# Kernel optimization log

Measured on AMD Instinct MI355X. Metric: run time of the kernel, lower is better.

## Reference

```python
import jax, jax.numpy as jnp
import numpy as np

B, N, TF, DM = 16, 4096, 512, 1024

def next_fast_len(n):
    # smallest 5-smooth number >= n (matches scipy.fftpack.next_fast_len)
    while True:
        m = n
        for p in (2, 3, 5):
            while m % p == 0:
                m //= p
        if m == 1:
            return n
        n += 1

def conv1d_fft(x, weights):
    # x: (..., N, F), weights: (M,); causal exponentially-weighted correlation
    n = x.shape[-2]
    m = weights.shape[-1]
    L = next_fast_len(n + m - 1)
    f_x = jnp.fft.rfft(x, n=L, axis=-2)                 # (..., Lr, F) complex
    f_w = jnp.fft.rfft(weights, n=L, axis=-1)           # (Lr,)
    out = jnp.fft.irfft(f_x * jnp.conj(f_w)[..., None], L, axis=-2)
    out = jnp.roll(out, -1, axis=-2)
    return out[..., L - n:, :]                           # last N along seq axis

def setup_inputs() -> dict:
    key = jax.random.key(0)
    ks = jax.random.split(key, 8)
    inp = {
        "x": jax.random.normal(ks[0], (B, N, TF), dtype=jnp.float32),
        "latent_growth": jax.random.normal(ks[1], (B, N, DM), dtype=jnp.float32),
        "latent_seasonal": jax.random.normal(ks[2], (B, N, DM), dtype=jnp.float32),
        "alpha": jnp.zeros((1,), dtype=jnp.float32),  # nn.Parameter(torch.Tensor([0.0]))
        "w_growth": jax.random.normal(ks[3], (TF, DM), dtype=jnp.float32) / np.sqrt(DM),
        "b_growth": jnp.zeros((TF,), dtype=jnp.float32),
        "w_seasonal": jax.random.normal(ks[4], (TF, DM), dtype=jnp.float32) / np.sqrt(DM),
        "b_seasonal": jnp.zeros((TF,), dtype=jnp.float32),
    }
    return inp

def reference(x, latent_growth, latent_seasonal, alpha, w_growth, b_growth, w_seasonal, b_seasonal):
    n = x.shape[1]
    a = jax.nn.sigmoid(alpha)[0]
    powers = jnp.arange(n, dtype=x.dtype)[::-1]          # flipped arange
    seasonal = jnp.einsum('bnd,fd->bnf', latent_seasonal, w_seasonal) + b_seasonal
    aes_weights = a * (1.0 - a) ** powers                # alpha*(1-alpha)^k EMA kernel
    seasonal_normalized_term = conv1d_fft(x - seasonal, aes_weights)
    # NOTE: the original module computes `growth` but does not use it in the output
    growth = jnp.einsum('bnd,fd->bnf', latent_growth, w_growth) + b_growth
    growth_term = conv1d_fft(x, aes_weights)
    return seasonal_normalized_term + growth_term
```

## Files before the change

### kernel.cpp

```cpp
#include <hip/hip_runtime.h>
#include <math.h>

#define B_DIM 16
#define N_SEQ 4096
#define TF_DIM 512
#define DM_DIM 1024
#define CHUNK 128
#define NCHUNK (N_SEQ / CHUNK)
#define NKT (DM_DIM / 32)

typedef __attribute__((ext_vector_type(4))) float f32x4;
typedef __attribute__((ext_vector_type(8))) short bf16x8;
typedef unsigned short u16;
typedef unsigned int u32;

__device__ __forceinline__ u16 f2bf(float f) {
    u32 u = __builtin_bit_cast(u32, f);
    u += 0x7fffu + ((u >> 16) & 1u);
    return (u16)(u >> 16);
}

__device__ __forceinline__ u32 cvtpk(float lo, float hi) {
    u32 r;
    asm("v_cvt_pk_bf16_f32 %0, %1, %2" : "=v"(r) : "v"(lo), "v"(hi));
    return r;
}

__device__ __forceinline__ void gload16(const u16* g, u16* l) {
    __builtin_amdgcn_global_load_lds(
        (const __attribute__((address_space(1))) void*)g,
        (__attribute__((address_space(3))) void*)l, 16, 0, 0);
}

#define SYNC_DRAIN() asm volatile("s_waitcnt vmcnt(0)\n\ts_barrier" ::: "memory")

__global__ __launch_bounds__(256)
void cvt_bf16(const float* __restrict__ ls, const float* __restrict__ wm,
              u16* __restrict__ lsb, u16* __restrict__ wmb)
{
    const size_t LSG = (size_t)B_DIM * N_SEQ * DM_DIM / 4;
    const size_t i = (size_t)blockIdx.x * 256 + threadIdx.x;
    const float* src;
    u16* dst;
    if (i < LSG) { src = ls + i * 4; dst = lsb + i * 4; }
    else         { const size_t j = i - LSG; src = wm + j * 4; dst = wmb + j * 4; }
    const f32x4 v = *(const f32x4*)src;
    u32* d = (u32*)dst;
    d[0] = cvtpk(v[0], v[1]);
    d[1] = cvtpk(v[2], v[3]);
}

__global__ __launch_bounds__(512, 4)
void gemm_u_kernel(const float* __restrict__ x,
                   const u16* __restrict__ lsb,
                   const u16* __restrict__ wmb,
                   const float* __restrict__ bias,
                   const float* __restrict__ alpha,
                   u16* __restrict__ u,
                   float* __restrict__ e)
{
    __shared__ u16 As[2][8192];
    __shared__ u16 Ws[2][4096];
    __shared__ float red[2][2][4][16];

    const int tid = threadIdx.x;

    const int s  = blockIdx.x;
    const int kk = s >> 3;
    const int fb = kk & 3;
    const int rp = (s & 7) + ((kk >> 2) << 3);
    const int f0   = fb * 128;
    const int row0 = rp * 256;

    const int lane = tid & 63;
    const int wid  = tid >> 6;
    const int wm = wid >> 1, wn = wid & 1;
    const int l15 = lane & 15, l4 = lane >> 4;

    const int srow = lane >> 2;
    const int sgc  = (lane & 3) ^ (srow & 3);
    const u16* pA = lsb + (size_t)(row0 + wid * 32 + srow) * DM_DIM + sgc * 8;
    const u16* pW = wmb + (size_t)(f0 + wid * 16 + srow) * DM_DIM + sgc * 8;

#define STAGE(BUF, KT) do {                                              \
        const int _o = (KT) * 32;                                        \
        gload16(pA + _o,                 &As[BUF][wid * 1024]);          \
        gload16(pA + _o + 16 * DM_DIM,   &As[BUF][wid * 1024 + 512]);    \
        gload16(pW + _o,                 &Ws[BUF][wid * 512]);           \
    } while (0)

    int rofa[4], rofw[4];
#pragma unroll
    for (int i = 0; i < 4; ++i) {
        const int ra = wm * 64 + i * 16 + l15;
        const int rw = wn * 64 + i * 16 + l15;
        rofa[i] = ra * 32 + ((l4 ^ (ra & 3)) * 8);
        rofw[i] = rw * 32 + ((l4 ^ (rw & 3)) * 8);
    }

    f32x4 acc[4][4];
#pragma unroll
    for (int i = 0; i < 4; ++i)
#pragma unroll
        for (int j = 0; j < 4; ++j) acc[i][j] = (f32x4){0.f, 0.f, 0.f, 0.f};

#define COMPUTE(BUF) do {                                                \
        const u16* _Ab = As[BUF];                                        \
        const u16* _Wb = Ws[BUF];                                        \
        bf16x8 _af[4], _wf[4];                                           \
        _Pragma("unroll")                                                \
        for (int i = 0; i < 4; ++i) {                                    \
            _af[i] = *(const bf16x8*)(_Ab + rofa[i]);                    \
            _wf[i] = *(const bf16x8*)(_Wb + rofw[i]);                    \
        }                                                                \
        _Pragma("unroll")                                                \
        for (int mi = 0; mi < 4; ++mi)                                   \
        _Pragma("unroll")                                                \
        for (int ni = 0; ni < 4; ++ni)                                   \
            acc[mi][ni] = __builtin_amdgcn_mfma_f32_16x16x32_bf16(       \
                _af[mi], _wf[ni], acc[mi][ni], 0, 0, 0);                 \
    } while (0)

    STAGE(0, 0);
    SYNC_DRAIN();

#pragma unroll 1
    for (int kt = 0; kt < NKT; kt += 2) {
        if (kt + 1 < NKT) STAGE(1, kt + 1);
        COMPUTE(0);
        SYNC_DRAIN();

        if (kt + 2 < NKT) STAGE(0, kt + 2);
        COMPUTE(1);
        SYNC_DRAIN();
    }

    const float a = 1.0f / (1.0f + expf(-alpha[0]));
    const float c = 1.0f - a;
    const float l2c = log2f(c);

    float bia[4];
#pragma unroll
    for (int ni = 0; ni < 4; ++ni) bia[ni] = bias[f0 + wn * 64 + ni * 16 + l15];

    float epart[4] = {0.f, 0.f, 0.f, 0.f};

#pragma unroll
    for (int mi = 0; mi < 4; ++mi) {
#pragma unroll
        for (int j = 0; j < 4; ++j) {
            const int r = wm * 64 + mi * 16 + l4 * 4 + j;
            const int rc = r & (CHUNK - 1);
            const size_t rb = (size_t)(row0 + r) * TF_DIM;
            const float wgt = (rc == CHUNK - 1)
                                  ? a
                                  : a * exp2f((float)(CHUNK - 1 - rc) * l2c);
#pragma unroll
            for (int ni = 0; ni < 4; ++ni) {
                const int f = f0 + wn * 64 + ni * 16 + l15;
                const float uval = 2.0f * x[rb + f] - (acc[mi][ni][j] + bia[ni]);
                u[rb + f] = f2bf(uval);
                epart[ni] = fmaf(wgt, uval, epart[ni]);
            }
        }
    }

#pragma unroll
    for (int ni = 0; ni < 4; ++ni) {
        epart[ni] += __shfl_xor(epart[ni], 16, 64);
        epart[ni] += __shfl_xor(epart[ni], 32, 64);
    }
    const int ch = wm >> 1;
    if ((wm & 1) == 1 && l4 == 0) {
#pragma unroll
        for (int ni = 0; ni < 4; ++ni) red[ch][wn][ni][l15] = epart[ni];
    }
    __syncthreads();
    if ((wm & 1) == 0 && l4 == 0) {
#pragma unroll
        for (int ni = 0; ni < 4; ++ni) {
            const int f = f0 + wn * 64 + ni * 16 + l15;
            e[(size_t)(rp * 2 + ch) * TF_DIM + f] = epart[ni] + red[ch][wn][ni][l15];
        }
    }
}

__global__ __launch_bounds__(256)
void ema_carry(const float* __restrict__ e, const float* __restrict__ alpha,
               float* __restrict__ carry)
{
    const int idx = blockIdx.x * 256 + threadIdx.x;
    const int f = idx & (TF_DIM - 1);
    const int b = idx >> 9;
    const float a = 1.0f / (1.0f + expf(-alpha[0]));
    const float c = 1.0f - a;
    const float cC = exp2f((float)CHUNK * log2f(c));
    const size_t base = (size_t)b * NCHUNK * TF_DIM + f;
    float Y = 0.0f;
    carry[base] = 0.0f;
    for (int ch = 1; ch < NCHUNK; ++ch) {
        Y = fmaf(cC, Y, e[base + (size_t)(ch - 1) * TF_DIM]);
        carry[base + (size_t)ch * TF_DIM] = Y;
    }
}

__global__ __launch_bounds__(256)
void ema_apply(const u16* __restrict__ u, const float* __restrict__ carry,
               const float* __restrict__ alpha, float* __restrict__ out)
{
    const int bc = blockIdx.x;
    const int tid = threadIdx.x;
    const float a = 1.0f / (1.0f + expf(-alpha[0]));
    const float c = 1.0f - a;
    float y0 = carry[(size_t)bc * TF_DIM + 2 * tid];
    float y1 = carry[(size_t)bc * TF_DIM + 2 * tid + 1];
    const u32* up = (const u32*)(u + (size_t)bc * CHUNK * TF_DIM) + tid;
    float2*    op = (float2*)(out + (size_t)bc * CHUNK * TF_DIM) + tid;
#pragma unroll 4
    for (int j = 0; j < CHUNK; ++j) {
        const u32 w = up[(size_t)j * (TF_DIM / 2)];
        const float u0 = __builtin_bit_cast(float, (w & 0xffffu) << 16);
        const float u1 = __builtin_bit_cast(float, (w >> 16) << 16);
        y0 = fmaf(c, y0, a * u0);
        y1 = fmaf(c, y1, a * u1);
        op[(size_t)j * (TF_DIM / 2)] = make_float2(y0, y1);
    }
}

extern "C" void kernel_launch(void* const* d_in, const int* in_sizes, int n_in,
                              void* d_out, int out_size, void* d_ws, size_t ws_size,
                              hipStream_t stream) {
    const float* x     = (const float*)d_in[0];
    const float* ls    = (const float*)d_in[2];
    const float* alpha = (const float*)d_in[3];
    const float* wmat  = (const float*)d_in[6];
    const float* bias  = (const float*)d_in[7];
    float* out = (float*)d_out;

    u16*   u     = (u16*)d_ws;
    u16*   lsb   = u + (size_t)B_DIM * N_SEQ * TF_DIM;
    u16*   wmb   = lsb + (size_t)B_DIM * N_SEQ * DM_DIM;
    float* e     = (float*)(wmb + (size_t)TF_DIM * DM_DIM);
    float* carry = e + (size_t)B_DIM * NCHUNK * TF_DIM;

    const int cvt_blocks = (B_DIM * N_SEQ * DM_DIM / 4 + TF_DIM * DM_DIM / 4) / 256;
    cvt_bf16<<<cvt_blocks, 256, 0, stream>>>(ls, wmat, lsb, wmb);

    gemm_u_kernel<<<1024, 512, 0, stream>>>(x, lsb, wmb, bias, alpha, u, e);

    ema_carry<<<(B_DIM * TF_DIM) / 256, 256, 0, stream>>>(e, alpha, carry);
    ema_apply<<<B_DIM * NCHUNK, 256, 0, stream>>>(u, carry, alpha, out);
}
```

Before: 244.4 us.

## Enlarge GEMM tile to 256x256 with K=64 stages and split-phase pipelining

The seasonal GEMM block tile grows from 256x128 to 256x256, with each wave computing 128x64 (8x4 MFMA tiles), and the K step doubles to 64, so the grid drops to 512 blocks. The aim is more operand reuse per byte loaded from LDS and global memory, fewer barriers per K, and better MFMA density. Staging of A and W is split across sub-phases with s_setprio around the MFMA bursts to overlap loads with compute. The epilogue reduction no longer goes through shared memory because each wave now covers a full 128-row chunk. The cost is higher register and LDS use (64KB), which lowers occupancy to 2 blocks per CU.

```diff
diff --git a/kernel.cpp b/kernel.cpp
--- a/kernel.cpp
+++ b/kernel.cpp
@@ -7,7 +7,7 @@
 #define DM_DIM 1024
 #define CHUNK 128
 #define NCHUNK (N_SEQ / CHUNK)
-#define NKT (DM_DIM / 32)
+#define NT 16
 
 typedef __attribute__((ext_vector_type(4))) float f32x4;
 typedef __attribute__((ext_vector_type(8))) short bf16x8;
@@ -32,6 +32,7 @@
         (__attribute__((address_space(3))) void*)l, 16, 0, 0);
 }
 
+#define BAR() __builtin_amdgcn_s_barrier()
 #define SYNC_DRAIN() asm volatile("s_waitcnt vmcnt(0)\n\ts_barrier" ::: "memory")
 
 __global__ __launch_bounds__(256)
@@ -50,7 +51,7 @@
     d[1] = cvtpk(v[2], v[3]);
 }
 
-__global__ __launch_bounds__(512, 4)
+__global__ __launch_bounds__(512, 2)
 void gemm_u_kernel(const float* __restrict__ x,
                    const u16* __restrict__ lsb,
                    const u16* __restrict__ wmb,
@@ -59,79 +60,100 @@
                    u16* __restrict__ u,
                    float* __restrict__ e)
 {
-    __shared__ u16 As[2][8192];
-    __shared__ u16 Ws[2][4096];
-    __shared__ float red[2][2][4][16];
+    __shared__ u16 As[2][2][8192];
+    __shared__ u16 Ws[2][2][8192];
 
     const int tid = threadIdx.x;
 
     const int s  = blockIdx.x;
     const int kk = s >> 3;
-    const int fb = kk & 3;
-    const int rp = (s & 7) + ((kk >> 2) << 3);
-    const int f0   = fb * 128;
+    const int fb = kk & 1;
+    const int rp = (s & 7) + ((kk >> 1) << 3);
+    const int f0   = fb * 256;
     const int row0 = rp * 256;
 
     const int lane = tid & 63;
     const int wid  = tid >> 6;
-    const int wm = wid >> 1, wn = wid & 1;
+    const int wm = wid >> 2;
+    const int wn = wid & 3;
+    const int wh = wn >> 1, wlo = wn & 1;
     const int l15 = lane & 15, l4 = lane >> 4;
 
-    const int srow = lane >> 2;
-    const int sgc  = (lane & 3) ^ (srow & 3);
-    const u16* pA = lsb + (size_t)(row0 + wid * 32 + srow) * DM_DIM + sgc * 8;
-    const u16* pW = wmb + (size_t)(f0 + wid * 16 + srow) * DM_DIM + sgc * 8;
-
-#define STAGE(BUF, KT) do {                                              \
-        const int _o = (KT) * 32;                                        \
-        gload16(pA + _o,                 &As[BUF][wid * 1024]);          \
-        gload16(pA + _o + 16 * DM_DIM,   &As[BUF][wid * 1024 + 512]);    \
-        gload16(pW + _o,                 &Ws[BUF][wid * 512]);           \
+    const int g0 = wid * 128 + lane;
+    const int g1 = g0 + 64;
+    const int r0 = ((g0 >> 7) << 4) | ((g0 >> 2) & 15);
+    const int c0 = (((g0 >> 6) & 1) << 5) | ((((g0 & 3) ^ (((g0 >> 5) & 1) << 1))) << 3);
+    const int r1 = ((g1 >> 7) << 4) | ((g1 >> 2) & 15);
+    const int c1 = (((g1 >> 6) & 1) << 5) | ((((g1 & 3) ^ (((g1 >> 5) & 1) << 1))) << 3);
+    const int dst0 = wid * 1024;
+    const int dst1 = wid * 1024 + 512;
+
+    const u16* pa0 = lsb + (size_t)(row0 + r0) * DM_DIM + c0;
+    const u16* pa1 = lsb + (size_t)(row0 + r1) * DM_DIM + c1;
+    const u16* pw0 = wmb + (size_t)(f0 + r0) * DM_DIM + c0;
+    const u16* pw1 = wmb + (size_t)(f0 + r1) * DM_DIM + c1;
+    const size_t H = (size_t)128 * DM_DIM;
+
+    const int com = (l15 << 5) | ((l4 << 3) ^ (((l15 >> 3) & 1) << 4));
+
+    f32x4 acc[8][4];
+#pragma unroll
+    for (int i = 0; i < 8; ++i)
+#pragma unroll
+        for (int j = 0; j < 4; ++j) acc[i][j] = (f32x4){0.f, 0.f, 0.f, 0.f};
+
+#define STAGE_A(NB, T) do {                                               \
+        gload16(pa0 + (size_t)(T) * 64,     &As[NB][0][dst0]);            \
+        gload16(pa1 + (size_t)(T) * 64,     &As[NB][0][dst1]);            \
+        gload16(pa0 + (size_t)(T) * 64 + H, &As[NB][1][dst0]);            \
+        gload16(pa1 + (size_t)(T) * 64 + H, &As[NB][1][dst1]);            \
     } while (0)
-
-    int rofa[4], rofw[4];
-#pragma unroll
-    for (int i = 0; i < 4; ++i) {
-        const int ra = wm * 64 + i * 16 + l15;
-        const int rw = wn * 64 + i * 16 + l15;
-        rofa[i] = ra * 32 + ((l4 ^ (ra & 3)) * 8);
-        rofw[i] = rw * 32 + ((l4 ^ (rw & 3)) * 8);
-    }
-
-    f32x4 acc[4][4];
-#pragma unroll
-    for (int i = 0; i < 4; ++i)
-#pragma unroll
-        for (int j = 0; j < 4; ++j) acc[i][j] = (f32x4){0.f, 0.f, 0.f, 0.f};
-
-#define COMPUTE(BUF) do {                                                \
-        const u16* _Ab = As[BUF];                                        \
-        const u16* _Wb = Ws[BUF];                                        \
-        bf16x8 _af[4], _wf[4];                                           \
-        _Pragma("unroll")                                                \
-        for (int i = 0; i < 4; ++i) {                                    \
-            _af[i] = *(const bf16x8*)(_Ab + rofa[i]);                    \
-            _wf[i] = *(const bf16x8*)(_Wb + rofw[i]);                    \
-        }                                                                \
-        _Pragma("unroll")                                                \
-        for (int mi = 0; mi < 4; ++mi)                                   \
-        _Pragma("unroll")                                                \
-        for (int ni = 0; ni < 4; ++ni)                                   \
-            acc[mi][ni] = __builtin_amdgcn_mfma_f32_16x16x32_bf16(       \
-                _af[mi], _wf[ni], acc[mi][ni], 0, 0, 0);                 \
+#define STAGE_W(NB, T) do {                                               \
+        gload16(pw0 + (size_t)(T) * 64,     &Ws[NB][0][dst0]);            \
+        gload16(pw1 + (size_t)(T) * 64,     &Ws[NB][0][dst1]);            \
+        gload16(pw0 + (size_t)(T) * 64 + H, &Ws[NB][1][dst0]);            \
+        gload16(pw1 + (size_t)(T) * 64 + H, &Ws[NB][1][dst1]);            \
     } while (0)
 
-    STAGE(0, 0);
+#define PHASE(BUF, MIH, KS) do {                                          \
+        const u16* _Ab = &As[BUF][wm][0];                                 \
+        const u16* _Wb = &Ws[BUF][wh][0];                                 \
+        bf16x8 _af[4], _wf[4];                                            \
+        _Pragma("unroll")                                                 \
+        for (int q = 0; q < 4; ++q)                                       \
+            _af[q] = *(const bf16x8*)(_Ab + (((MIH)*4 + q) << 10)         \
+                                          + ((KS) << 9) + com);           \
+        _Pragma("unroll")                                                 \
+        for (int n = 0; n < 4; ++n)                                       \
+            _wf[n] = *(const bf16x8*)(_Wb + ((wlo*4 + n) << 10)           \
+                                          + ((KS) << 9) + com);           \
+        __builtin_amdgcn_s_setprio(1);                                    \
+        _Pragma("unroll")                                                 \
+        for (int q = 0; q < 4; ++q)                                       \
+        _Pragma("unroll")                                                 \
+        for (int n = 0; n < 4; ++n)                                       \
+            acc[(MIH)*4 + q][n] = __builtin_amdgcn_mfma_f32_16x16x32_bf16(\
+                _af[q], _wf[n], acc[(MIH)*4 + q][n], 0, 0, 0);            \
+        __builtin_amdgcn_s_setprio(0);                                    \
+    } while (0)
+
+    STAGE_A(0, 0);
+    STAGE_W(0, 0);
     SYNC_DRAIN();
 
 #pragma unroll 1
-    for (int kt = 0; kt < NKT; kt += 2) {
-        if (kt + 1 < NKT) STAGE(1, kt + 1);
-        COMPUTE(0);
-        SYNC_DRAIN();
-
-        if (kt + 2 < NKT) STAGE(0, kt + 2);
-        COMPUTE(1);
+    for (int t = 0; t < NT; ++t) {
+        const int bt = t & 1;
+        const int nb = bt ^ 1;
+        if (t + 1 < NT) STAGE_A(nb, t + 1);
+        PHASE(bt, 0, 0);
+        BAR();
+        if (t + 1 < NT) STAGE_W(nb, t + 1);
+        PHASE(bt, 0, 1);
+        BAR();
+        PHASE(bt, 1, 0);
+        BAR();
+        PHASE(bt, 1, 1);
         SYNC_DRAIN();
     }
 
@@ -146,11 +168,11 @@
     float epart[4] = {0.f, 0.f, 0.f, 0.f};
 
 #pragma unroll
-    for (int mi = 0; mi < 4; ++mi) {
+    for (int mi = 0; mi < 8; ++mi) {
 #pragma unroll
         for (int j = 0; j < 4; ++j) {
-            const int r = wm * 64 + mi * 16 + l4 * 4 + j;
-            const int rc = r & (CHUNK - 1);
+            const int rc = mi * 16 + l4 * 4 + j;
+            const int r  = wm * 128 + rc;
             const size_t rb = (size_t)(row0 + r) * TF_DIM;
             const float wgt = (rc == CHUNK - 1)
                                   ? a
@@ -170,17 +192,11 @@
         epart[ni] += __shfl_xor(epart[ni], 16, 64);
         epart[ni] += __shfl_xor(epart[ni], 32, 64);
     }
-    const int ch = wm >> 1;
-    if ((wm & 1) == 1 && l4 == 0) {
-#pragma unroll
-        for (int ni = 0; ni < 4; ++ni) red[ch][wn][ni][l15] = epart[ni];
-    }
-    __syncthreads();
-    if ((wm & 1) == 0 && l4 == 0) {
+    if (l4 == 0) {
 #pragma unroll
         for (int ni = 0; ni < 4; ++ni) {
             const int f = f0 + wn * 64 + ni * 16 + l15;
-            e[(size_t)(rp * 2 + ch) * TF_DIM + f] = epart[ni] + red[ch][wn][ni][l15];
+            e[(size_t)(rp * 2 + wm) * TF_DIM + f] = epart[ni];
         }
     }
 }
@@ -246,7 +262,7 @@
     const int cvt_blocks = (B_DIM * N_SEQ * DM_DIM / 4 + TF_DIM * DM_DIM / 4) / 256;
     cvt_bf16<<<cvt_blocks, 256, 0, stream>>>(ls, wmat, lsb, wmb);
 
-    gemm_u_kernel<<<1024, 512, 0, stream>>>(x, lsb, wmb, bias, alpha, u, e);
+    gemm_u_kernel<<<512, 512, 0, stream>>>(x, lsb, wmb, bias, alpha, u, e);
 
     ema_carry<<<(B_DIM * TF_DIM) / 256, 256, 0, stream>>>(e, alpha, carry);
     ema_apply<<<B_DIM * NCHUNK, 256, 0, stream>>>(u, carry, alpha, out);
```

New measurement: 247.5 us. No clear change (+1.3%).
